# Kernel tuning notes

Measured on AMD Instinct MI355X. Metric: run time of the kernel, lower is better.

The kernel has to match this reference:

```python
import jax, jax.numpy as jnp
import numpy as np

B, D, C = 512, 16384, 3
SAMPLE_DURATION = 16
NEG_THRESHOLD = 0.5
NEGPOS_RATIO = 3


def setup_inputs() -> dict:
    key = jax.random.key(0)
    k1, k2, k3, k4, k5, k6, k7 = jax.random.split(key, 7)
    loc_pred = jax.random.normal(k1, (B, D, 2), dtype=jnp.float32)
    conf_pred = jax.random.normal(k2, (B, D, C), dtype=jnp.float32)
    # one ground-truth (start, end, label) per sample, within [0, 16]
    start = jax.random.uniform(k3, (B,), dtype=jnp.float32) * 8.0
    length = 1.0 + jax.random.uniform(k4, (B,), dtype=jnp.float32) * 7.0
    label = jax.random.randint(k5, (B,), 0, C).astype(jnp.float32)
    targets = jnp.stack([start, start + length, label], axis=-1)  # [B,3]
    # default bars stored as (center, length) in frame units
    centers = 1.0 + jax.random.uniform(k6, (D,), dtype=jnp.float32) * (SAMPLE_DURATION - 2.0)
    lengths = 1.0 + jax.random.uniform(k7, (D,), dtype=jnp.float32) * (SAMPLE_DURATION - 4.0)
    default_bar = jnp.stack([centers, lengths], axis=-1)  # [D,2]
    return {"loc_pred": loc_pred, "conf_pred": conf_pred,
            "targets": targets, "default_bar": default_bar}


def _match_one(truth, label, default):
    """truth [2]=(start,end), label scalar int, default [D,2]=(center,length).
    Returns loc_t [D,2], conf_t [D] (0=ignore, 1=background, >1=fg)."""
    d_c, d_l = default[:, 0], default[:, 1]
    d_s, d_e = d_c - d_l * 0.5, d_c + d_l * 0.5
    inter = jnp.clip(jnp.minimum(truth[1], d_e) - jnp.maximum(truth[0], d_s), 0.0)
    union = (truth[1] - truth[0]) + (d_e - d_s) - inter
    ov = inter / union                                   # [D] 1-D IoU
    best_prior = jnp.argmax(ov)                          # best anchor for the truth
    bto = ov.at[best_prior].set(2.0)                     # index_fill_ with 2
    conf = jnp.full((D,), label + 1, dtype=jnp.int32)    # single truth -> broadcast
    is_bg = conf == 1
    conf = jnp.where(bto < NEG_THRESHOLD, 0, conf)
    conf = jnp.where(is_bg, 1, conf)
    # SSD-style encoding of matched (start,end) against (center,length)
    m_c = (truth[0] + truth[1]) * 0.5
    m_l = truth[1] - truth[0]
    loc = jnp.stack([(m_c - d_c) / d_l, jnp.log(m_l / d_l)], axis=-1)  # [D,2]
    return loc, conf


def reference(loc_pred, conf_pred, targets, default_bar):
    truths = targets[:, :2]                              # [B,2]
    labels = targets[:, 2].astype(jnp.int32)             # [B]
    loc_t, conf_t = jax.vmap(_match_one, in_axes=(0, 0, None))(truths, labels, default_bar)
    loc_t = jax.lax.stop_gradient(loc_t)                 # built under no_grad in torch
    conf_t = jax.lax.stop_gradient(conf_t)

    pos = conf_t > 0                                     # [B,D] used for mining
    loc_pos = conf_t > 1                                 # [B,D] used for loc loss

    # SmoothL1 (beta=1), reduction='sum' over positives
    diff = loc_pred - loc_t
    ad = jnp.abs(diff)
    sl1 = jnp.where(ad < 1.0, 0.5 * diff * diff, ad - 0.5)
    loss_loc = jnp.sum(sl1 * loc_pos[..., None].astype(sl1.dtype))

    # hard-negative mining on per-anchor CE surrogate
    conf_tc = jnp.clip(conf_t - 1, 0)                    # [B,D] class ids 0..C-1
    lse = jax.nn.logsumexp(conf_pred, axis=-1)           # [B,D]
    gathered = jnp.take_along_axis(conf_pred, conf_tc[..., None], axis=-1)[..., 0]
    lc = lse - gathered
    lc = jnp.where(pos, 0.0, lc)
    loss_idx = jnp.argsort(-lc, axis=1)                  # descending sort
    idx_rank = jnp.argsort(loss_idx, axis=1)
    num_pos = jnp.sum(pos.astype(jnp.int32), axis=1, keepdims=True)   # [B,1]
    num_neg = jnp.clip(NEGPOS_RATIO * num_pos, max=D - 1)
    neg = idx_rank < num_neg                             # [B,D]

    sel = (pos | neg).astype(conf_pred.dtype)
    logp = jax.nn.log_softmax(conf_pred, axis=-1)
    ce = -jnp.take_along_axis(logp, conf_tc[..., None], axis=-1)[..., 0]
    loss_conf = jnp.sum(ce * sel)

    N = jnp.sum(num_pos).astype(loss_loc.dtype)
    return jnp.stack([loss_loc / N, loss_conf / N])
```

## Files before the change

### kernel.cpp

```cpp
#include <hip/hip_runtime.h>
#include <hip/hip_fp16.h>
#include <math.h>

constexpr int Bn = 512;
constexpr int Dn = 16384;
constexpr int BS = 512;
constexpr int CHUNKS = 4;
constexpr int CPRI = Dn / CHUNKS;
constexpr int K1T = 256;
constexpr int WT = 4;
constexpr int TP = 256;

__device__ __forceinline__ float lse3(float a, float b, float c) {
  float m = fmaxf(a, fmaxf(b, c));
  return m + __logf(__expf(a - m) + __expf(b - m) + __expf(c - m));
}
__device__ __forceinline__ float sl1f(float x) {
  float a = fabsf(x);
  return a < 1.f ? 0.5f * x * x : a - 0.5f;
}

__device__ __forceinline__ double blockReduceAddD(double v, double* sred) {
  int t = threadIdx.x;
  sred[t] = v;
  __syncthreads();
  for (int off = BS >> 1; off > 0; off >>= 1) {
    if (t < off) sred[t] += sred[t + off];
    __syncthreads();
  }
  double r = sred[0];
  __syncthreads();
  return r;
}

#define WAITV(n) do { asm volatile("s_waitcnt vmcnt(" #n ")" ::: "memory"); \
                      __builtin_amdgcn_sched_barrier(0); } while (0)
#define WAITL()  do { asm volatile("s_waitcnt lgkmcnt(0)" ::: "memory"); \
                      __builtin_amdgcn_sched_barrier(0); } while (0)

__global__ __launch_bounds__(K1T) void multiloss_stream(
    const float* __restrict__ loc_pred, const float* __restrict__ conf_pred,
    const float* __restrict__ targets, const float* __restrict__ default_bar,
    unsigned* __restrict__ lc32,
    float* __restrict__ pce, float* __restrict__ plloc, int* __restrict__ pnpos)
{
  __shared__ float s_lds[4 * 2 * 1280];

  const int bid = blockIdx.x;
  const int b = bid >> 2, c = bid & 3;
  const int t = threadIdx.x;
  const int l = t & 63, w = t >> 6;

  float4* wbuf = (float4*)(s_lds + w * 2560);

  const float4* __restrict__ confs =
      (const float4*)conf_pred + (size_t)b * 12288 + c * 3072 + w * 768;
  const float4* __restrict__ bars =
      (const float4*)default_bar + c * 2048 + w * 512;

  auto stage = [&](int buf, int tile) {
    const float4* cs = confs + tile * 192;
    float4* cd = wbuf + buf * 320;
    #pragma unroll
    for (int j = 0; j < 3; ++j)
      __builtin_amdgcn_global_load_lds(
          (const __attribute__((address_space(1))) void*)(cs + j * 64 + l),
          (__attribute__((address_space(3))) void*)(cd + j * 64), 16, 0, 0);
    const float4* bs = bars + tile * 128;
    float4* bd = cd + 192;
    #pragma unroll
    for (int j = 0; j < 2; ++j)
      __builtin_amdgcn_global_load_lds(
          (const __attribute__((address_space(1))) void*)(bs + j * 64 + l),
          (__attribute__((address_space(3))) void*)(bd + j * 64), 16, 0, 0);
  };

  stage(0, 0);
  stage(1, 1);

  const float t0  = targets[b * 3 + 0];
  const float t1  = targets[b * 3 + 1];
  const int   lab = (int)targets[b * 3 + 2];

  float ce = 0.f, lloc = 0.f; int npos = 0;
  const float m_c = (t0 + t1) * 0.5f;
  const float T   = t1 - t0;

  if (lab == 0) {
    auto consume0 = [&](int buf) {
      const float4* cd = wbuf + buf * 320;
      float4 cA = cd[3 * l], cB = cd[3 * l + 1], cC = cd[3 * l + 2];
      const float cf[12] = {cA.x, cA.y, cA.z, cA.w, cB.x, cB.y, cB.z, cB.w, cC.x, cC.y, cC.z, cC.w};
      #pragma unroll
      for (int i = 0; i < 4; ++i) {
        float x = cf[3 * i], y = cf[3 * i + 1], z = cf[3 * i + 2];
        float hi = fmaxf(x, y), lo = fminf(x, y);
        float m  = fmaxf(hi, z), mid = fminf(hi, z);
        float s  = 1.f + __expf(lo - m) + __expf(mid - m);
        ce += (m - x) + __logf(s);
      }
    };
    WAITV(5); consume0(0); WAITL(); stage(0, 2);
    WAITV(5); consume0(1); WAITL(); stage(1, 3);
    WAITV(5); consume0(0);
    WAITV(0); consume0(1);
  } else {
    const float log_ml = __logf(T);
    const float2* __restrict__ lp2 =
        (const float2*)loc_pred + (size_t)b * Dn + c * CPRI + w * 1024;
    unsigned* __restrict__ lcbase = lc32 + (size_t)b * 8192 + (c * CPRI + w * 1024) / 2;

    auto consume = [&](int buf, int tile) {
      const float4* cd = wbuf + buf * 320;
      const float4* bd = cd + 192;
      float4 cA = cd[3 * l], cB = cd[3 * l + 1], cC = cd[3 * l + 2];
      float4 b0 = bd[2 * l], b1 = bd[2 * l + 1];
      const float cf[12] = {cA.x, cA.y, cA.z, cA.w, cB.x, cB.y, cB.z, cB.w, cC.x, cC.y, cC.z, cC.w};
      const float bf[8]  = {b0.x, b0.y, b0.z, b0.w, b1.x, b1.y, b1.z, b1.w};
      float lcv[4];
      const int gbase = tile * TP + 4 * l;
      #pragma unroll
      for (int i = 0; i < 4; ++i) {
        float x = cf[3 * i], y = cf[3 * i + 1], z = cf[3 * i + 2];
        float dc = bf[2 * i], dl = bf[2 * i + 1];
        float ds = __fmaf_rn(-0.5f, dl, dc);
        float de = __fmaf_rn(0.5f, dl, dc);
        float inter = fmaxf(fminf(t1, de) - fmaxf(t0, ds), 0.f);
        float uni = (T + dl) - inter;
        bool pos = (2.f * inter >= uni);
        float hi = fmaxf(x, y), lo = fminf(x, y);
        float m  = fmaxf(hi, z), mid = fminf(hi, z);
        float s  = 1.f + __expf(lo - m) + __expf(mid - m);
        float lnS = __logf(s);
        float cl = (lab == 1) ? y : z;
        npos += pos;
        ce += pos ? ((m - cl) + lnS) : 0.f;
        lcv[i] = pos ? 0.f : ((m - x) + lnS);
        if (pos) {
          float2 lp = lp2[gbase + i];
          float pd0 = lp.x - __fdividef(m_c - dc, dl);
          float pd1 = (lp.y - log_ml) + __logf(dl);
          lloc += sl1f(pd0) + sl1f(pd1);
        }
      }
      __half2 h0 = __floats2half2_rn(lcv[0], lcv[1]);
      __half2 h1 = __floats2half2_rn(lcv[2], lcv[3]);
      uint2 pk = make_uint2(*reinterpret_cast<unsigned*>(&h0),
                            *reinterpret_cast<unsigned*>(&h1));
      ((uint2*)(lcbase + tile * (TP / 2)))[l] = pk;
    };
    WAITV(5); consume(0, 0); WAITL(); stage(0, 2);
    WAITV(6); consume(1, 1); WAITL(); stage(1, 3);
    WAITV(6); consume(0, 2);
    WAITV(1); consume(1, 3);
  }

  #pragma unroll
  for (int off = 1; off < 64; off <<= 1) {
    ce   += __shfl_xor(ce, off);
    lloc += __shfl_xor(lloc, off);
    npos += __shfl_xor(npos, off);
  }
  __syncthreads();
  float* red = s_lds;
  if (l == 0) {
    red[w * 3 + 0] = ce; red[w * 3 + 1] = lloc; red[w * 3 + 2] = __int_as_float(npos);
  }
  __syncthreads();
  if (t == 0) {
    float Ce = 0.f, Ll = 0.f; int Np = 0;
    #pragma unroll
    for (int k = 0; k < 4; ++k) {
      Ce += red[k * 3 + 0]; Ll += red[k * 3 + 1]; Np += __float_as_int(red[k * 3 + 2]);
    }
    int pidx = b * CHUNKS + c;
    pce[pidx] = Ce; plloc[pidx] = Ll; pnpos[pidx] = Np;
  }
}

__global__ __launch_bounds__(BS) void multiloss_select(
    const float* __restrict__ loc_pred, const float* __restrict__ conf_pred,
    const float* __restrict__ targets, const float* __restrict__ default_bar,
    const unsigned short* __restrict__ lc16,
    const float* __restrict__ pce, const float* __restrict__ plloc,
    const int* __restrict__ pnpos,
    double* __restrict__ rloc, double* __restrict__ rconf, double* __restrict__ rnp)
{
  __shared__ unsigned short s_lc[Dn];
  __shared__ int      s_hist[256];
  __shared__ double   s_dred[BS];
  __shared__ float    s_fv[BS];
  __shared__ int      s_fi[BS];
  __shared__ unsigned s_wt[8];
  __shared__ unsigned s_sel[2];
  __shared__ double   s_sc[2];
  __shared__ int      s_np;

  const int b = blockIdx.x;
  const int t = threadIdx.x;
  const int lab = (int)targets[b * 3 + 2];

  if (lab == 0) {
    if (t == 0) {
      double ce = 0.0;
      for (int kk = 0; kk < CHUNKS; ++kk) ce += (double)pce[CHUNKS * b + kk];
      rloc[b] = 0.0; rconf[b] = ce; rnp[b] = (double)Dn;
    }
    return;
  }

  const float t0 = targets[b * 3 + 0];
  const float t1 = targets[b * 3 + 1];

  const float4* lcr = (const float4*)(lc16 + (size_t)b * Dn);
  float4* sl4 = (float4*)s_lc;
  #pragma unroll
  for (int j = 0; j < Dn / 8 / BS; ++j) sl4[j * BS + t] = lcr[j * BS + t];
  __syncthreads();

  if (t == 0) {
    double ce = 0.0, ll = 0.0; int np = 0;
    for (int kk = 0; kk < CHUNKS; ++kk) {
      int pi = CHUNKS * b + kk;
      ce += (double)pce[pi]; ll += (double)plloc[pi]; np += pnpos[pi];
    }
    s_sc[0] = ce; s_sc[1] = ll; s_np = np;
  }
  __syncthreads();
  int np = s_np;

  if (np == 0) {
    float bV = -1.f; int bI = 0;
    for (int d = t; d < Dn; d += BS) {
      float2 db = ((const float2*)default_bar)[d];
      float d_s = db.x - db.y * 0.5f;
      float d_e = db.x + db.y * 0.5f;
      float inter = fmaxf(fminf(t1, d_e) - fmaxf(t0, d_s), 0.f);
      float uni = (t1 - t0) + (d_e - d_s) - inter;
      float ov = inter / uni;
      if (ov > bV) { bV = ov; bI = d; }
    }
    s_fv[t] = bV; s_fi[t] = bI;
    __syncthreads();
    for (int off = BS >> 1; off > 0; off >>= 1) {
      if (t < off) {
        float v2 = s_fv[t + off]; int i2 = s_fi[t + off];
        if (v2 > s_fv[t] || (v2 == s_fv[t] && i2 < s_fi[t])) { s_fv[t] = v2; s_fi[t] = i2; }
      }
      __syncthreads();
    }
    if (t == 0) {
      int d = s_fi[0];
      const float* cp = conf_pred + (size_t)b * Dn * 3 + (size_t)d * 3;
      float c0 = cp[0], c1 = cp[1], c2 = cp[2];
      float lse = lse3(c0, c1, c2);
      float cl = (lab == 1) ? c1 : c2;
      float2 db = ((const float2*)default_bar)[d];
      float2 lp = ((const float2*)loc_pred)[(size_t)b * Dn + d];
      float m_c = (t0 + t1) * 0.5f, m_l = t1 - t0;
      float pd0 = lp.x - (m_c - db.x) / db.y;
      float pd1 = lp.y - __logf(m_l / db.y);
      s_sc[0] += (double)(lse - cl);
      s_sc[1] += (double)(sl1f(pd0) + sl1f(pd1));
      s_np = 1;
      s_lc[d] = 0;
    }
    __syncthreads();
    np = s_np;
  }
  const int k = min(3 * np, Dn - 1);

  unsigned prefix = 0;
  int K = k;
  const int lane = t & 63, w = t >> 6;
  for (int r = 0; r < 2; ++r) {
    if (t < 256) s_hist[t] = 0;
    __syncthreads();
    for (int d = t; d < Dn; d += BS) {
      unsigned u = s_lc[d];
      bool ok = (r == 0) || ((u >> 8) == prefix);
      if (ok) {
        unsigned bin = (r == 0) ? (u >> 8) : (u & 0xFFu);
        atomicAdd(&s_hist[bin], 1);
      }
    }
    __syncthreads();
    unsigned psum = (t < 256) ? (unsigned)s_hist[t] : 0u;
    unsigned incl = psum;
    #pragma unroll
    for (int off = 1; off < 64; off <<= 1) {
      unsigned v = __shfl_down(incl, off, 64);
      if (lane + off < 64) incl += v;
    }
    if (lane == 0) s_wt[w] = incl;
    __syncthreads();
    unsigned aboveW = 0;
    for (int w2 = w + 1; w2 < 8; ++w2) aboveW += s_wt[w2];
    const unsigned above = aboveW + (incl - psum);
    if (t < 256 && above < (unsigned)K && (unsigned)K <= above + psum) {
      s_sel[0] = (unsigned)t;
      s_sel[1] = above;
    }
    __syncthreads();
    unsigned selBin = s_sel[0];
    K -= (int)s_sel[1];
    prefix = (r == 0) ? selBin : ((prefix << 8) | selBin);
    __syncthreads();
  }
  const unsigned tb = prefix;

  float    ssum = 0.f;
  unsigned scnt = 0;
  for (int d = t; d < Dn; d += BS) {
    unsigned u = s_lc[d];
    if (u > tb) {
      ssum += __half2float(__ushort_as_half((unsigned short)u));
      scnt++;
    }
  }
  double S = blockReduceAddD((double)ssum, s_dred);
  double C = blockReduceAddD((double)scnt, s_dred);

  if (t == 0) {
    double tval = (double)__half2float(__ushort_as_half((unsigned short)tb));
    double topk = S + ((double)k - C) * tval;
    rloc[b]  = s_sc[1];
    rconf[b] = s_sc[0] + topk;
    rnp[b]   = (double)np;
  }
}

__global__ __launch_bounds__(BS) void multiloss_mono(
    const float* __restrict__ loc_pred, const float* __restrict__ conf_pred,
    const float* __restrict__ targets, const float* __restrict__ default_bar,
    double* __restrict__ rloc, double* __restrict__ rconf, double* __restrict__ rnp)
{
  __shared__ float    s_lc[Dn];
  __shared__ int      s_hist[2048];
  __shared__ unsigned s_scan[BS];
  __shared__ double   s_dred[BS];
  __shared__ unsigned s_sel[2];
  __shared__ double   s_corr[2];
  __shared__ int      s_np;

  const int b = blockIdx.x;
  const int t = threadIdx.x;

  const float t0  = targets[b * 3 + 0];
  const float t1  = targets[b * 3 + 1];
  const int   lab = (int)targets[b * 3 + 2];

  const float* __restrict__ cpb = conf_pred + (size_t)b * Dn * 3;

  if (lab == 0) {
    float ce = 0.f;
    for (int d = t; d < Dn; d += BS) {
      const float* cp = cpb + d * 3;
      ce += lse3(cp[0], cp[1], cp[2]) - cp[0];
    }
    double tot = blockReduceAddD((double)ce, s_dred);
    if (t == 0) { rloc[b] = 0.0; rconf[b] = tot; rnp[b] = (double)Dn; }
    return;
  }

  const float m_c = (t0 + t1) * 0.5f;
  const float m_l = t1 - t0;

  float bestV = -1.f; int bestI = 0;
  int   nposL = 0;
  float cePosL = 0.f;
  float llocL  = 0.f;

  for (int d = t; d < Dn; d += BS) {
    float2 db = ((const float2*)default_bar)[d];
    float d_c = db.x, d_l = db.y;
    float d_s = d_c - d_l * 0.5f;
    float d_e = d_c + d_l * 0.5f;
    float inter = fmaxf(fminf(t1, d_e) - fmaxf(t0, d_s), 0.f);
    float uni = (t1 - t0) + (d_e - d_s) - inter;
    float ov  = inter / uni;

    const float* cp = cpb + d * 3;
    float c0 = cp[0];
    float lse = lse3(cp[0], cp[1], cp[2]);

    if (ov > bestV) { bestV = ov; bestI = d; }

    float lcv;
    if (ov >= 0.5f) {
      nposL++;
      float cl = (lab == 1) ? cp[1] : cp[2];
      cePosL += lse - cl;
      float2 lp = ((const float2*)loc_pred)[(size_t)b * Dn + d];
      float pd0 = lp.x - (m_c - d_c) / d_l;
      float pd1 = lp.y - __logf(m_l / d_l);
      llocL += sl1f(pd0) + sl1f(pd1);
      lcv = 0.f;
    } else {
      lcv = lse - c0;
    }
    s_lc[d] = lcv;
  }

  float* sv = (float*)s_hist;
  int*   si = (int*)(s_hist + BS);
  sv[t] = bestV; si[t] = bestI;
  __syncthreads();
  for (int off = BS >> 1; off > 0; off >>= 1) {
    if (t < off) {
      float v2 = sv[t + off]; int i2 = si[t + off];
      if (v2 > sv[t] || (v2 == sv[t] && i2 < si[t])) { sv[t] = v2; si[t] = i2; }
    }
    __syncthreads();
  }
  float bV = sv[0]; int bI = si[0];
  __syncthreads();

  double nposTot  = blockReduceAddD((double)nposL, s_dred);
  double cePosTot = blockReduceAddD((double)cePosL, s_dred);
  double llocTot  = blockReduceAddD((double)llocL, s_dred);
  int num_pos = (int)(nposTot + 0.5);

  if (t == 0) {
    double cc = 0.0, lcor = 0.0; int np2 = num_pos;
    if (bV < 0.5f) {
      int d = bI;
      const float* cp = cpb + d * 3;
      float lse = lse3(cp[0], cp[1], cp[2]);
      float cl = (lab == 1) ? cp[1] : cp[2];
      cc = (double)(lse - cl);
      float2 db = ((const float2*)default_bar)[d];
      float2 lp = ((const float2*)loc_pred)[(size_t)b * Dn + d];
      float pd0 = lp.x - (m_c - db.x) / db.y;
      float pd1 = lp.y - __logf(m_l / db.y);
      lcor = (double)(sl1f(pd0) + sl1f(pd1));
      np2 += 1;
      s_lc[d] = 0.f;
    }
    s_corr[0] = cc; s_corr[1] = lcor; s_np = np2;
  }
  __syncthreads();
  int np = s_np;
  int k  = min(3 * np, Dn - 1);

  unsigned prefix = 0;
  int K = k;
  for (int r = 0; r < 3; ++r) {
    for (int i = t; i < 2048; i += BS) s_hist[i] = 0;
    __syncthreads();
    for (int d = t; d < Dn; d += BS) {
      unsigned u = __float_as_uint(s_lc[d]);
      bool ok = (r == 0) || (r == 1 ? ((u >> 21) == prefix) : ((u >> 10) == prefix));
      if (ok) {
        unsigned bin = (r == 0) ? (u >> 21)
                     : (r == 1) ? ((u >> 10) & 0x7FFu)
                                : (u & 0x3FFu);
        atomicAdd(&s_hist[bin], 1);
      }
    }
    __syncthreads();
    int nb  = (r == 2) ? 1024 : 2048;
    int per = nb / BS;
    unsigned psum = 0;
    for (int j = 0; j < per; ++j) psum += (unsigned)s_hist[t * per + j];
    s_scan[t] = psum;
    __syncthreads();
    for (int off = 1; off < BS; off <<= 1) {
      unsigned v = (t + off < BS) ? s_scan[t + off] : 0u;
      __syncthreads();
      s_scan[t] += v;
      __syncthreads();
    }
    unsigned above = (t < BS - 1) ? s_scan[t + 1] : 0u;
    if (above < (unsigned)K && (unsigned)K <= above + psum) {
      unsigned cum = above;
      int found = 0;
      for (int j = per - 1; j >= 0; --j) {
        unsigned c = (unsigned)s_hist[t * per + j];
        if (cum + c >= (unsigned)K) { found = j; break; }
        cum += c;
      }
      s_sel[0] = (unsigned)(t * per + found);
      s_sel[1] = cum;
    }
    __syncthreads();
    unsigned selBin = s_sel[0];
    K -= (int)s_sel[1];
    prefix = (r == 0) ? selBin
           : (r == 1) ? ((prefix << 11) | selBin)
                      : ((prefix << 10) | selBin);
    __syncthreads();
  }
  const unsigned tb = prefix;

  float    ssum = 0.f;
  unsigned scnt = 0;
  for (int d = t; d < Dn; d += BS) {
    float v = s_lc[d];
    if (__float_as_uint(v) > tb) { ssum += v; scnt++; }
  }
  double S = blockReduceAddD((double)ssum, s_dred);
  double C = blockReduceAddD((double)scnt, s_dred);

  if (t == 0) {
    double tval = (double)__uint_as_float(tb);
    double topk = S + ((double)k - C) * tval;
    rloc[b]  = llocTot + s_corr[1];
    rconf[b] = cePosTot + s_corr[0] + topk;
    rnp[b]   = (double)s_np;
  }
}

__global__ __launch_bounds__(512) void multiloss_final(
    const double* __restrict__ rloc, const double* __restrict__ rconf,
    const double* __restrict__ rnp, float* __restrict__ out)
{
  __shared__ double s1[512], s2[512], s3[512];
  int t = threadIdx.x;
  s1[t] = rloc[t];
  s2[t] = rconf[t];
  s3[t] = rnp[t];
  __syncthreads();
  for (int off = 256; off > 0; off >>= 1) {
    if (t < off) { s1[t] += s1[t + off]; s2[t] += s2[t + off]; s3[t] += s3[t + off]; }
    __syncthreads();
  }
  if (t == 0) {
    double N = s3[0];
    out[0] = (float)(s1[0] / N);
    out[1] = (float)(s2[0] / N);
  }
}

extern "C" void kernel_launch(void* const* d_in, const int* in_sizes, int n_in,
                              void* d_out, int out_size, void* d_ws, size_t ws_size,
                              hipStream_t stream) {
  const float* loc_pred    = (const float*)d_in[0];
  const float* conf_pred   = (const float*)d_in[1];
  const float* targets     = (const float*)d_in[2];
  const float* default_bar = (const float*)d_in[3];
  float* out = (float*)d_out;
  char* ws = (char*)d_ws;

  constexpr size_t LC_BYTES = (size_t)Bn * Dn * sizeof(unsigned short);
  constexpr size_t P_CNT = (size_t)Bn * CHUNKS;
  size_t off = LC_BYTES;
  float*  pce   = (float*)(ws + off); off += P_CNT * 4;
  float*  plloc = (float*)(ws + off); off += P_CNT * 4;
  int*    pnpos = (int*)(ws + off);   off += P_CNT * 4;
  double* rloc  = (double*)(ws + off); off += Bn * 8;
  double* rconf = (double*)(ws + off); off += Bn * 8;
  double* rnp   = (double*)(ws + off); off += Bn * 8;
  const size_t NEED = off;

  if (ws_size >= NEED) {
    hipLaunchKernelGGL(multiloss_stream, dim3(Bn * CHUNKS), dim3(K1T), 0, stream,
                       loc_pred, conf_pred, targets, default_bar,
                       (unsigned*)ws, pce, plloc, pnpos);
    hipLaunchKernelGGL(multiloss_select, dim3(Bn), dim3(BS), 0, stream,
                       loc_pred, conf_pred, targets, default_bar,
                       (const unsigned short*)ws, pce, plloc, pnpos,
                       rloc, rconf, rnp);
    hipLaunchKernelGGL(multiloss_final, dim3(1), dim3(512), 0, stream,
                       rloc, rconf, rnp, out);
  } else {
    double* mloc  = (double*)ws;
    double* mconf = mloc + Bn;
    double* mnp   = mconf + Bn;
    hipLaunchKernelGGL(multiloss_mono, dim3(Bn), dim3(BS), 0, stream,
                       loc_pred, conf_pred, targets, default_bar, mloc, mconf, mnp);
    hipLaunchKernelGGL(multiloss_final, dim3(1), dim3(512), 0, stream,
                       mloc, mconf, mnp, out);
  }
}
```

Baseline: 63.44 us.

## Replace LDS double-buffered streaming with direct register loads across more blocks

The streaming kernel drops its global-to-LDS double-buffer pipeline and instead has each thread load its 4 anchors' conf and bar data straight into registers. The grid goes from 4 to 16 blocks per sample so that more blocks in flight hide latency instead of manual vmcnt pipelining. The log-sum-exp is also simplified to an unshifted sum of exps, which removes the max/min work but can overflow for large logits. The select kernel must read partials with the new CHUNKS value, and the shared constant covers that.

```diff
diff --git a/kernel.cpp b/kernel.cpp
--- a/kernel.cpp
+++ b/kernel.cpp
@@ -5,11 +5,9 @@
 constexpr int Bn = 512;
 constexpr int Dn = 16384;
 constexpr int BS = 512;
-constexpr int CHUNKS = 4;
+constexpr int CHUNKS = 16;
 constexpr int CPRI = Dn / CHUNKS;
 constexpr int K1T = 256;
-constexpr int WT = 4;
-constexpr int TP = 256;
 
 __device__ __forceinline__ float lse3(float a, float b, float c) {
   float m = fmaxf(a, fmaxf(b, c));
@@ -32,11 +30,6 @@
   __syncthreads();
   return r;
 }
-
-#define WAITV(n) do { asm volatile("s_waitcnt vmcnt(" #n ")" ::: "memory"); \
-                      __builtin_amdgcn_sched_barrier(0); } while (0)
-#define WAITL()  do { asm volatile("s_waitcnt lgkmcnt(0)" ::: "memory"); \
-                      __builtin_amdgcn_sched_barrier(0); } while (0)
 
 __global__ __launch_bounds__(K1T) void multiloss_stream(
     const float* __restrict__ loc_pred, const float* __restrict__ conf_pred,
@@ -44,39 +37,20 @@
     unsigned* __restrict__ lc32,
     float* __restrict__ pce, float* __restrict__ plloc, int* __restrict__ pnpos)
 {
-  __shared__ float s_lds[4 * 2 * 1280];
+  __shared__ float s_red[12];
 
   const int bid = blockIdx.x;
-  const int b = bid >> 2, c = bid & 3;
+  const int b = bid >> 4, c = bid & 15;
   const int t = threadIdx.x;
   const int l = t & 63, w = t >> 6;
 
-  float4* wbuf = (float4*)(s_lds + w * 2560);
-
-  const float4* __restrict__ confs =
-      (const float4*)conf_pred + (size_t)b * 12288 + c * 3072 + w * 768;
-  const float4* __restrict__ bars =
-      (const float4*)default_bar + c * 2048 + w * 512;
-
-  auto stage = [&](int buf, int tile) {
-    const float4* cs = confs + tile * 192;
-    float4* cd = wbuf + buf * 320;
-    #pragma unroll
-    for (int j = 0; j < 3; ++j)
-      __builtin_amdgcn_global_load_lds(
-          (const __attribute__((address_space(1))) void*)(cs + j * 64 + l),
-          (__attribute__((address_space(3))) void*)(cd + j * 64), 16, 0, 0);
-    const float4* bs = bars + tile * 128;
-    float4* bd = cd + 192;
-    #pragma unroll
-    for (int j = 0; j < 2; ++j)
-      __builtin_amdgcn_global_load_lds(
-          (const __attribute__((address_space(1))) void*)(bs + j * 64 + l),
-          (__attribute__((address_space(3))) void*)(bd + j * 64), 16, 0, 0);
-  };
-
-  stage(0, 0);
-  stage(1, 1);
+  const int p0 = c * CPRI + 4 * t;
+
+  const float4* cp4 = (const float4*)(conf_pred + (size_t)b * Dn * 3 + (size_t)p0 * 3);
+  const float4* bp4 = (const float4*)(default_bar + (size_t)p0 * 2);
+  float4 C0 = cp4[0], C1 = cp4[1], C2 = cp4[2];
+  float4 B0 = bp4[0], B1 = bp4[1];
+  __builtin_amdgcn_sched_barrier(0);
 
   const float t0  = targets[b * 3 + 0];
   const float t1  = targets[b * 3 + 1];
@@ -86,73 +60,47 @@
   const float m_c = (t0 + t1) * 0.5f;
   const float T   = t1 - t0;
 
+  const float cf[12] = {C0.x, C0.y, C0.z, C0.w, C1.x, C1.y, C1.z, C1.w, C2.x, C2.y, C2.z, C2.w};
+  const float bf[8]  = {B0.x, B0.y, B0.z, B0.w, B1.x, B1.y, B1.z, B1.w};
+
   if (lab == 0) {
-    auto consume0 = [&](int buf) {
-      const float4* cd = wbuf + buf * 320;
-      float4 cA = cd[3 * l], cB = cd[3 * l + 1], cC = cd[3 * l + 2];
-      const float cf[12] = {cA.x, cA.y, cA.z, cA.w, cB.x, cB.y, cB.z, cB.w, cC.x, cC.y, cC.z, cC.w};
-      #pragma unroll
-      for (int i = 0; i < 4; ++i) {
-        float x = cf[3 * i], y = cf[3 * i + 1], z = cf[3 * i + 2];
-        float hi = fmaxf(x, y), lo = fminf(x, y);
-        float m  = fmaxf(hi, z), mid = fminf(hi, z);
-        float s  = 1.f + __expf(lo - m) + __expf(mid - m);
-        ce += (m - x) + __logf(s);
-      }
-    };
-    WAITV(5); consume0(0); WAITL(); stage(0, 2);
-    WAITV(5); consume0(1); WAITL(); stage(1, 3);
-    WAITV(5); consume0(0);
-    WAITV(0); consume0(1);
+    #pragma unroll
+    for (int i = 0; i < 4; ++i) {
+      float x = cf[3 * i], y = cf[3 * i + 1], z = cf[3 * i + 2];
+      float s = __expf(x) + __expf(y) + __expf(z);
+      ce += __logf(s) - x;
+    }
   } else {
     const float log_ml = __logf(T);
-    const float2* __restrict__ lp2 =
-        (const float2*)loc_pred + (size_t)b * Dn + c * CPRI + w * 1024;
-    unsigned* __restrict__ lcbase = lc32 + (size_t)b * 8192 + (c * CPRI + w * 1024) / 2;
-
-    auto consume = [&](int buf, int tile) {
-      const float4* cd = wbuf + buf * 320;
-      const float4* bd = cd + 192;
-      float4 cA = cd[3 * l], cB = cd[3 * l + 1], cC = cd[3 * l + 2];
-      float4 b0 = bd[2 * l], b1 = bd[2 * l + 1];
-      const float cf[12] = {cA.x, cA.y, cA.z, cA.w, cB.x, cB.y, cB.z, cB.w, cC.x, cC.y, cC.z, cC.w};
-      const float bf[8]  = {b0.x, b0.y, b0.z, b0.w, b1.x, b1.y, b1.z, b1.w};
-      float lcv[4];
-      const int gbase = tile * TP + 4 * l;
-      #pragma unroll
-      for (int i = 0; i < 4; ++i) {
-        float x = cf[3 * i], y = cf[3 * i + 1], z = cf[3 * i + 2];
-        float dc = bf[2 * i], dl = bf[2 * i + 1];
-        float ds = __fmaf_rn(-0.5f, dl, dc);
-        float de = __fmaf_rn(0.5f, dl, dc);
-        float inter = fmaxf(fminf(t1, de) - fmaxf(t0, ds), 0.f);
-        float uni = (T + dl) - inter;
-        bool pos = (2.f * inter >= uni);
-        float hi = fmaxf(x, y), lo = fminf(x, y);
-        float m  = fmaxf(hi, z), mid = fminf(hi, z);
-        float s  = 1.f + __expf(lo - m) + __expf(mid - m);
-        float lnS = __logf(s);
-        float cl = (lab == 1) ? y : z;
-        npos += pos;
-        ce += pos ? ((m - cl) + lnS) : 0.f;
-        lcv[i] = pos ? 0.f : ((m - x) + lnS);
-        if (pos) {
-          float2 lp = lp2[gbase + i];
-          float pd0 = lp.x - __fdividef(m_c - dc, dl);
-          float pd1 = (lp.y - log_ml) + __logf(dl);
-          lloc += sl1f(pd0) + sl1f(pd1);
-        }
+    const float2* __restrict__ lp2 = (const float2*)loc_pred + (size_t)b * Dn;
+    float lcv[4];
+    #pragma unroll
+    for (int i = 0; i < 4; ++i) {
+      float x = cf[3 * i], y = cf[3 * i + 1], z = cf[3 * i + 2];
+      float dc = bf[2 * i], dl = bf[2 * i + 1];
+      float ds = __fmaf_rn(-0.5f, dl, dc);
+      float de = __fmaf_rn(0.5f, dl, dc);
+      float inter = fmaxf(fminf(t1, de) - fmaxf(t0, ds), 0.f);
+      float uni = (T + dl) - inter;
+      bool pos = (2.f * inter >= uni);
+      float s = __expf(x) + __expf(y) + __expf(z);
+      float lse = __logf(s);
+      float cl = (lab == 1) ? y : z;
+      npos += pos;
+      ce += pos ? (lse - cl) : 0.f;
+      lcv[i] = pos ? 0.f : (lse - x);
+      if (pos) {
+        float2 lp = lp2[p0 + i];
+        float pd0 = lp.x - __fdividef(m_c - dc, dl);
+        float pd1 = (lp.y - log_ml) + __logf(dl);
+        lloc += sl1f(pd0) + sl1f(pd1);
       }
-      __half2 h0 = __floats2half2_rn(lcv[0], lcv[1]);
-      __half2 h1 = __floats2half2_rn(lcv[2], lcv[3]);
-      uint2 pk = make_uint2(*reinterpret_cast<unsigned*>(&h0),
-                            *reinterpret_cast<unsigned*>(&h1));
-      ((uint2*)(lcbase + tile * (TP / 2)))[l] = pk;
-    };
-    WAITV(5); consume(0, 0); WAITL(); stage(0, 2);
-    WAITV(6); consume(1, 1); WAITL(); stage(1, 3);
-    WAITV(6); consume(0, 2);
-    WAITV(1); consume(1, 3);
+    }
+    __half2 h0 = __floats2half2_rn(lcv[0], lcv[1]);
+    __half2 h1 = __floats2half2_rn(lcv[2], lcv[3]);
+    uint2 pk = make_uint2(*reinterpret_cast<unsigned*>(&h0),
+                          *reinterpret_cast<unsigned*>(&h1));
+    *((uint2*)(lc32 + ((size_t)b * Dn + p0) / 2)) = pk;
   }
 
   #pragma unroll
@@ -161,17 +109,15 @@
     lloc += __shfl_xor(lloc, off);
     npos += __shfl_xor(npos, off);
   }
-  __syncthreads();
-  float* red = s_lds;
   if (l == 0) {
-    red[w * 3 + 0] = ce; red[w * 3 + 1] = lloc; red[w * 3 + 2] = __int_as_float(npos);
+    s_red[w * 3 + 0] = ce; s_red[w * 3 + 1] = lloc; s_red[w * 3 + 2] = __int_as_float(npos);
   }
   __syncthreads();
   if (t == 0) {
     float Ce = 0.f, Ll = 0.f; int Np = 0;
     #pragma unroll
     for (int k = 0; k < 4; ++k) {
-      Ce += red[k * 3 + 0]; Ll += red[k * 3 + 1]; Np += __float_as_int(red[k * 3 + 2]);
+      Ce += s_red[k * 3 + 0]; Ll += s_red[k * 3 + 1]; Np += __float_as_int(s_red[k * 3 + 2]);
     }
     int pidx = b * CHUNKS + c;
     pce[pidx] = Ce; plloc[pidx] = Ll; pnpos[pidx] = Np;
```

Result: faster. 57.73 us, median of 2 (-9.0%).
